# Optimization experiments

Hardware: AMD Instinct MI355X
Metric: run time of the kernel (lower is better)

## Reference

```python
import jax, jax.numpy as jnp
import numpy as np

D = 256; NH = 8; HD = D // NH; FF = 1024; NLAYERS = 6
REG_MAX = 32; NBIN = REG_MAX + 1; NC = 80; KQ = 4
SPATIAL = [(80, 80), (40, 40), (20, 20)]; NPTS = [4, 4, 4]; SUMP = sum(NPTS)
LQ = 300; B = 16; OFFSET_SCALE = 0.5; UP = 0.5; REG_SCALE = 4.0
TOT = NH * SUMP


def _project_np():
    ub1 = abs(UP) * abs(REG_SCALE); ub2 = ub1 * 2
    step = (ub1 + 1.0) ** (2.0 / (REG_MAX - 2))
    left = [-(step ** i) + 1 for i in range(REG_MAX // 2 - 1, 0, -1)]
    right = [step ** i - 1 for i in range(1, REG_MAX // 2)]
    return np.array([-ub2] + left + [0.0] + right + [ub2], dtype=np.float32)

PROJ_NP = _project_np()  # [NBIN]


def layer_norm(x, g, b):
    mu = x.mean(-1, keepdims=True)
    var = ((x - mu) ** 2).mean(-1, keepdims=True)
    return (x - mu) * jax.lax.rsqrt(var + 1e-5) * g + b


def inv_sigmoid(x, eps=1e-5):
    x = jnp.clip(x, eps, 1.0 - eps)
    return jnp.log(x) - jnp.log1p(-x)


def mlp2(x, w1, b1, w2, b2):
    return jax.nn.silu(x @ w1 + b1) @ w2 + b2


def mlp3(x, w1, b1, w2, b2, w3, b3):
    return jax.nn.silu(jax.nn.silu(x @ w1 + b1) @ w2 + b2) @ w3 + b3


def grid_sample(img, grid):
    # bilinear, padding_mode='zeros', align_corners=False. img [N,C,H,W], grid [N,Hg,Wg,2] in [-1,1]
    N, C, H, W = img.shape
    gshape = grid.shape[1:3]
    x = (grid[..., 0] + 1.0) * (W * 0.5) - 0.5
    y = (grid[..., 1] + 1.0) * (H * 0.5) - 0.5
    x0f = jnp.floor(x); y0f = jnp.floor(y)
    wx = x - x0f; wy = y - y0f
    x0 = x0f.astype(jnp.int32); y0 = y0f.astype(jnp.int32)
    imgf = img.reshape(N, C, H * W)
    def tap(xi, yi, wt):
        valid = ((xi >= 0) & (xi < W) & (yi >= 0) & (yi < H)).astype(img.dtype)
        idx = jnp.clip(yi, 0, H - 1) * W + jnp.clip(xi, 0, W - 1)
        v = jnp.take_along_axis(imgf, idx.reshape(N, 1, -1), axis=2).reshape(N, C, gshape[0], gshape[1])
        return v * (valid * wt)[:, None]
    return (tap(x0, y0, (1 - wx) * (1 - wy)) + tap(x0 + 1, y0, wx * (1 - wy))
            + tap(x0, y0 + 1, (1 - wx) * wy) + tap(x0 + 1, y0 + 1, wx * wy))


def self_attention(q_in, k_in, v_in, qw, qb, kw, kb, vw, vb, ow, ob):
    q = (q_in @ qw + qb).reshape(B, LQ, NH, HD)
    k = (k_in @ kw + kb).reshape(B, LQ, NH, HD)
    v = (v_in @ vw + vb).reshape(B, LQ, NH, HD)
    a = jax.nn.softmax(jnp.einsum('bqhd,bkhd->bhqk', q, k) * (HD ** -0.5), -1)
    o = jnp.einsum('bhqk,bkhd->bqhd', a, v).reshape(B, LQ, D)
    return o @ ow + ob


def distance2bbox(points, distance):
    rs = abs(REG_SCALE); half = 0.5 * rs
    x1 = points[..., 0] - (half + distance[..., 0]) * (points[..., 2] / rs)
    y1 = points[..., 1] - (half + distance[..., 1]) * (points[..., 3] / rs)
    x2 = points[..., 0] + (half + distance[..., 2]) * (points[..., 2] / rs)
    y2 = points[..., 1] + (half + distance[..., 3]) * (points[..., 3] / rs)
    return jnp.stack([(x1 + x2) * 0.5, (y1 + y2) * 0.5, x2 - x1, y2 - y1], -1)


def lqe_head(scores, corners, w1, b1, w2, b2):
    prob = jax.nn.softmax(corners.reshape(B, LQ, 4, NBIN), -1)
    topk, _ = jax.lax.top_k(prob, KQ)                         # [B,LQ,4,KQ]
    stat = jnp.concatenate([topk, topk.mean(-1, keepdims=True)], -1)  # [B,LQ,4,KQ+1]
    return scores + mlp2(stat.reshape(B, LQ, 4 * (KQ + 1)), w1, b1, w2, b2)


def reference(target, ref_pts_unact, memory,
              sa_qw, sa_qb, sa_kw, sa_kb, sa_vw, sa_vb, sa_ow, sa_ob,
              n1_g, n1_b, off_w, off_b, aw_w, aw_b,
              gate_w, gate_b, gn_g, gn_b,
              ff1_w, ff1_b, ff2_w, ff2_b, n3_g, n3_b,
              bb_w1, bb_b1, bb_w2, bb_b2, bb_w3, bb_b3,
              sc_w, sc_b, lqe_w1, lqe_b1, lqe_w2, lqe_b2,
              qp_w1, qp_b1, qp_w2, qp_b2,
              pb_w1, pb_b1, pb_w2, pb_b2, pb_w3, pb_b3):
    project = jnp.asarray(PROJ_NP)
    # --- value prep: memory [B,S,D] -> per-level [B*NH, HD, h, w] ---
    val = memory.reshape(B, -1, NH, HD).transpose(0, 2, 3, 1).reshape(B * NH, HD, -1)
    splits = np.cumsum([h * w for h, w in SPATIAL])[:-1].tolist()
    value_lvls = [v.reshape(B * NH, HD, h, w)
                  for v, (h, w) in zip(jnp.split(val, splits, axis=2), SPATIAL)]
    nps = jnp.asarray(np.repeat(1.0 / np.array(NPTS, np.float32), NPTS))  # [SUMP]

    ref_pts = jax.nn.sigmoid(ref_pts_unact)
    output = target
    out_prev = jnp.zeros_like(target)
    corners_prev = jnp.zeros((B, LQ, 4 * NBIN), dtype=target.dtype)
    ref_init = ref_pts
    final_logits = final_bboxes = None

    for i in range(NLAYERS):
        qp = jnp.clip(mlp2(ref_pts, qp_w1, qp_b1, qp_w2, qp_b2), -10.0, 10.0)
        # self attention
        q = output + qp
        t2 = self_attention(q, q, output, sa_qw[i], sa_qb[i], sa_kw[i], sa_kb[i],
                            sa_vw[i], sa_vb[i], sa_ow[i], sa_ob[i])
        output = layer_norm(output + t2, n1_g[i], n1_b[i])
        # deformable cross attention
        qc = output + qp
        offs = (qc @ off_w[i] + off_b[i]).reshape(B, LQ, NH, SUMP, 2)
        attnw = jax.nn.softmax((qc @ aw_w[i] + aw_b[i]).reshape(B, LQ, NH, SUMP), -1)
        offset = offs * nps[:, None] * ref_pts[:, :, None, None, 2:] * OFFSET_SCALE
        locs = ref_pts[:, :, None, None, :2] + offset            # [B,LQ,NH,SUMP,2]
        grids = (2.0 * locs - 1.0).transpose(0, 2, 1, 3, 4).reshape(B * NH, LQ, SUMP, 2)
        p0 = 0; sampled = []
        for lvl in range(len(SPATIAL)):
            sampled.append(grid_sample(value_lvls[lvl], grids[:, :, p0:p0 + NPTS[lvl]]))
            p0 += NPTS[lvl]
        samp = jnp.concatenate(sampled, -1)                      # [B*NH, HD, LQ, SUMP]
        aw = attnw.transpose(0, 2, 1, 3).reshape(B * NH, 1, LQ, SUMP)
        t2 = (samp * aw).sum(-1).reshape(B, D, LQ).transpose(0, 2, 1)
        # gateway
        g12 = jax.nn.sigmoid(jnp.concatenate([output, t2], -1) @ gate_w[i] + gate_b[i])
        output = layer_norm(g12[..., :D] * output + g12[..., D:] * t2, gn_g[i], gn_b[i])
        # FFN
        t2 = jax.nn.relu(output @ ff1_w[i] + ff1_b[i]) @ ff2_w[i] + ff2_b[i]
        output = layer_norm(jnp.clip(output + t2, -65504.0, 65504.0), n3_g[i], n3_b[i])
        # FDR box refinement
        if i == 0:
            pre_bb = jax.nn.sigmoid(mlp3(output, pb_w1, pb_b1, pb_w2, pb_b2, pb_w3, pb_b3)
                                    + inv_sigmoid(ref_pts))
            ref_init = pre_bb
        corners = mlp3(output + out_prev, bb_w1[i], bb_b1[i], bb_w2[i], bb_b2[i],
                       bb_w3[i], bb_b3[i]) + corners_prev
        dist = jax.nn.softmax(corners.reshape(B, LQ, 4, NBIN), -1) @ project  # [B,LQ,4]
        inter = distance2bbox(ref_init, dist)
        if i == NLAYERS - 1:  # eval_idx
            scores = output @ sc_w[i] + sc_b[i]
            final_logits = lqe_head(scores, corners, lqe_w1[i], lqe_b1[i], lqe_w2[i], lqe_b2[i])
            final_bboxes = inter
        corners_prev = corners
        ref_pts = inter
        out_prev = output
    return jnp.concatenate([final_bboxes, final_logits], -1)  # [B, LQ, 4+NC]


def setup_inputs() -> dict:
    key = jax.random.key(0)
    cnt = [0]
    def rnd(shape, scale=0.02):
        cnt[0] += 1
        return jax.random.normal(jax.random.fold_in(key, cnt[0]), shape, dtype=jnp.float32) * scale
    S = sum(h * w for h, w in SPATIAL)
    L = NLAYERS
    return {
        'target': rnd((B, LQ, D), 1.0),
        'ref_pts_unact': rnd((B, LQ, 4), 1.0),
        'memory': rnd((B, S, D), 1.0),
        'sa_qw': rnd((L, D, D)), 'sa_qb': rnd((L, D)),
        'sa_kw': rnd((L, D, D)), 'sa_kb': rnd((L, D)),
        'sa_vw': rnd((L, D, D)), 'sa_vb': rnd((L, D)),
        'sa_ow': rnd((L, D, D)), 'sa_ob': rnd((L, D)),
        'n1_g': jnp.ones((L, D)), 'n1_b': jnp.zeros((L, D)),
        'off_w': rnd((L, D, TOT * 2)), 'off_b': rnd((L, TOT * 2)),
        'aw_w': rnd((L, D, TOT)), 'aw_b': rnd((L, TOT)),
        'gate_w': rnd((L, 2 * D, 2 * D)), 'gate_b': rnd((L, 2 * D)),
        'gn_g': jnp.ones((L, D)), 'gn_b': jnp.zeros((L, D)),
        'ff1_w': rnd((L, D, FF)), 'ff1_b': rnd((L, FF)),
        'ff2_w': rnd((L, FF, D)), 'ff2_b': rnd((L, D)),
        'n3_g': jnp.ones((L, D)), 'n3_b': jnp.zeros((L, D)),
        'bb_w1': rnd((L, D, D)), 'bb_b1': rnd((L, D)),
        'bb_w2': rnd((L, D, D)), 'bb_b2': rnd((L, D)),
        'bb_w3': rnd((L, D, 4 * NBIN)), 'bb_b3': rnd((L, 4 * NBIN)),
        'sc_w': rnd((L, D, NC)), 'sc_b': rnd((L, NC)),
        'lqe_w1': rnd((L, 4 * (KQ + 1), 64)), 'lqe_b1': rnd((L, 64)),
        'lqe_w2': rnd((L, 64, 1)), 'lqe_b2': rnd((L, 1)),
        'qp_w1': rnd((4, 2 * D)), 'qp_b1': rnd((2 * D,)),
        'qp_w2': rnd((2 * D, D)), 'qp_b2': rnd((D,)),
        'pb_w1': rnd((D, D)), 'pb_b1': rnd((D,)),
        'pb_w2': rnd((D, D)), 'pb_b2': rnd((D,)),
        'pb_w3': rnd((D, 4)), 'pb_b3': rnd((4,)),
    }
```

## Files before the change

### kernel.cpp

```cpp
#include <hip/hip_runtime.h>
#include <cstddef>
#include <cmath>
#include <utility>

#define B_ 16
#define LQ_ 300
#define D_ 256
#define NH_ 8
#define HD_ 32
#define FF_ 1024
#define NBIN_ 33
#define NC_ 80
#define SUMP_ 12
#define STOT_ 8400
#define R_ (B_*LQ_)
#define NLAYERS_ 6

typedef short bf16x8 __attribute__((ext_vector_type(8)));
typedef float f32x4  __attribute__((ext_vector_type(4)));

static __device__ __forceinline__ short f2bf(float x) {
  union { float f; unsigned u; } v; v.f = x;
  unsigned r = v.u + 0x7fffu + ((v.u >> 16) & 1u);
  return (short)(r >> 16);
// ... 155 lines not shown
      bf16x8 ab0 = *(const bf16x8*)(obp0 + k0 + lq * 8);
      bf16x8 ab1 = *(const bf16x8*)(obp1 + k0 + lq * 8);
      #pragma unroll
      for (int t = 0; t < 6; ++t) {
        bf16x8 w = *(const bf16x8*)(Qt + (size_t)(cbase + t * 16 + lr) * 256 + k0 + lq * 8);
        bool useoq = (cbase + t * 16) < 512;
        acc[0][t] = __builtin_amdgcn_mfma_f32_16x16x32_bf16(useoq ? aq0 : ab0, w, acc[0][t], 0, 0, 0);
        acc[1][t] = __builtin_amdgcn_mfma_f32_16x16x32_bf16(useoq ? aq1 : ab1, w, acc[1][t], 0, 0, 0);
      }
    }
    #pragma unroll
    for (int t = 0; t < 6; ++t) {
      int colt = cbase + t * 16 + lr;
      float bv = qkvbias[colt];
      #pragma unroll
      for (int ti = 0; ti < 2; ++ti)
        #pragma unroll
        for (int rr = 0; rr < 4; ++rr)
          qkvout[(size_t)(m0 + ti * 16 + lq * 4 + rr) * 768 + colt] = f2bf(acc[ti][t][rr] + bv);
    }
  }
}

__launch_bounds__(512)
__global__ void sow_ln_off(const short* __restrict__ A, const short* __restrict__ Wt,
                           const float* __restrict__ bias, const float* __restrict__ resid,
                           const float* __restrict__ gamma, const float* __restrict__ beta,
                           const float* __restrict__ qp,
                           const short* __restrict__ OWt, const float* __restrict__ ob,
                           float* __restrict__ outf, short* __restrict__ outbf,
                           float* __restrict__ offout) {
  __shared__ float ssum[32][8];
  __shared__ float ssq[32][8];
  __shared__ short oqs[32][264];
  const int m0 = blockIdx.x * 32;
  const int tid = threadIdx.x, wid = tid >> 6, lane = tid & 63;
  const int lr = lane & 15, lq = lane >> 4;
  const int cw = wid * 32;
  f32x4 acc[2][2];
  #pragma unroll
  for (int ti = 0; ti < 2; ++ti)
    #pragma unroll
    for (int t = 0; t < 2; ++t) acc[ti][t] = (f32x4){0.f, 0.f, 0.f, 0.f};
  #pragma unroll
  for (int k0 = 0; k0 < 256; k0 += 32) {
    bf16x8 a0 = *(const bf16x8*)(A + (size_t)(m0 + lr) * 256 + k0 + lq * 8);
    bf16x8 a1 = *(const bf16x8*)(A + (size_t)(m0 + 16 + lr) * 256 + k0 + lq * 8);
    #pragma unroll
    for (int t = 0; t < 2; ++t) {
      bf16x8 w = *(const bf16x8*)(Wt + (size_t)(cw + t * 16 + lr) * 256 + k0 + lq * 8);
      acc[0][t] = __builtin_amdgcn_mfma_f32_16x16x32_bf16(a0, w, acc[0][t], 0, 0, 0);
      acc[1][t] = __builtin_amdgcn_mfma_f32_16x16x32_bf16(a1, w, acc[1][t], 0, 0, 0);
    }
  }
  float s[2][4], q[2][4];
  #pragma unroll
  for (int ti = 0; ti < 2; ++ti)
    #pragma unroll
    for (int rr = 0; rr < 4; ++rr) { s[ti][rr] = 0.f; q[ti][rr] = 0.f; }
  #pragma unroll
  for (int t = 0; t < 2; ++t) {
    int col = cw + t * 16 + lr;
    float bv = bias[col];
    #pragma unroll
    for (int ti = 0; ti < 2; ++ti)
      #pragma unroll
      for (int rr = 0; rr < 4; ++rr) {
        int rowg = m0 + ti * 16 + lq * 4 + rr;
        float x = acc[ti][t][rr] + bv + resid[(size_t)rowg * 256 + col];
        acc[ti][t][rr] = x;
        s[ti][rr] += x; q[ti][rr] += x * x;
      }
  }
  #pragma unroll
  for (int m = 1; m < 16; m <<= 1)
    #pragma unroll
    for (int ti = 0; ti < 2; ++ti)
      #pragma unroll
      for (int rr = 0; rr < 4; ++rr) {
        s[ti][rr] += __shfl_xor(s[ti][rr], m);
        q[ti][rr] += __shfl_xor(q[ti][rr], m);
      }
  if (lr == 0)
    #pragma unroll
    for (int ti = 0; ti < 2; ++ti)
      #pragma unroll
      for (int rr = 0; rr < 4; ++rr) {
        ssum[ti * 16 + lq * 4 + rr][wid] = s[ti][rr];
        ssq[ti * 16 + lq * 4 + rr][wid] = q[ti][rr];
      }
  __syncthreads();
  float mu[2][4], rs[2][4];
  #pragma unroll
  for (int ti = 0; ti < 2; ++ti)
    #pragma unroll
    for (int rr = 0; rr < 4; ++rr) {
      int rl = ti * 16 + lq * 4 + rr;
      float sm = 0.f, sq = 0.f;
      #pragma unroll
      for (int w8 = 0; w8 < 8; ++w8) { sm += ssum[rl][w8]; sq += ssq[rl][w8]; }
      float m_ = sm * (1.f / 256.f);
      float var = sq * (1.f / 256.f) - m_ * m_;
      mu[ti][rr] = m_; rs[ti][rr] = rsqrtf(var + 1e-5f);
    }
  #pragma unroll
  for (int t = 0; t < 2; ++t) {
    int col = cw + t * 16 + lr;
    float g = gamma[col], be = beta[col];
    #pragma unroll
    for (int ti = 0; ti < 2; ++ti)
      #pragma unroll
      for (int rr = 0; rr < 4; ++rr) {
        int rl = ti * 16 + lq * 4 + rr;
        size_t idx = (size_t)(m0 + rl) * 256 + col;
        float v = (acc[ti][t][rr] - mu[ti][rr]) * rs[ti][rr] * g + be;
        outf[idx] = v;
        outbf[idx] = f2bf(v);
        oqs[rl][col] = f2bf(v + qp[idx]);
      }
  }
  __syncthreads();
  f32x4 oacc[2][3];
  #pragma unroll
  for (int ti = 0; ti < 2; ++ti)
    #pragma unroll
    for (int j = 0; j < 3; ++j) oacc[ti][j] = (f32x4){0.f, 0.f, 0.f, 0.f};
  #pragma unroll 4
  for (int k0 = 0; k0 < 256; k0 += 32) {
    bf16x8 a0 = *(const bf16x8*)&oqs[lr][k0 + lq * 8];
    bf16x8 a1 = *(const bf16x8*)&oqs[16 + lr][k0 + lq * 8];
    #pragma unroll
    for (int j = 0; j < 3; ++j) {
      int tile = wid + j * 8;
      int trow = (tile < 18) ? tile * 16 + lr : 0;
      bf16x8 w = *(const bf16x8*)(OWt + (size_t)trow * 256 + k0 + lq * 8);
      oacc[0][j] = __builtin_amdgcn_mfma_f32_16x16x32_bf16(a0, w, oacc[0][j], 0, 0, 0);
      oacc[1][j] = __builtin_amdgcn_mfma_f32_16x16x32_bf16(a1, w, oacc[1][j], 0, 0, 0);
    }
  }
  #pragma unroll
  for (int j = 0; j < 3; ++j) {
    int tile = wid + j * 8;
    if (tile >= 18) continue;
    int col = tile * 16 + lr;
    float bv = ob[col];
    #pragma unroll
    for (int ti = 0; ti < 2; ++ti)
      #pragma unroll
      for (int rr = 0; rr < 4; ++rr)
        offout[(size_t)(m0 + ti * 16 + lq * 4 + rr) * 288 + col] = oacc[ti][j][rr] + bv;
  }
}

template<int SCORES>
__launch_bounds__(512)
__global__ void ffn_ln(const short* __restrict__ A, const short* __restrict__ W1t,
                       const float* __restrict__ b1, const short* __restrict__ W2t,
                       const float* __restrict__ b2, const float* __restrict__ resid,
                       const float* __restrict__ gamma, const float* __restrict__ beta,
                       float* __restrict__ prev, float* __restrict__ outf,
                       short* __restrict__ outbf, short* __restrict__ oqbf,
                       const short* __restrict__ SCt, const float* __restrict__ scb,
                       float* __restrict__ scoresOut) {
  __shared__ short hid[32][1032];
  __shared__ float ssum[32][8];
  __shared__ float ssq[32][8];
  const int m0 = blockIdx.x * 32;
  const int tid = threadIdx.x, wid = tid >> 6, lane = tid & 63;
  const int lr = lane & 15, lq = lane >> 4;
  {
    f32x4 acc[2][8];
    #pragma unroll
    for (int ti = 0; ti < 2; ++ti)
      #pragma unroll
      for (int t = 0; t < 8; ++t) acc[ti][t] = (f32x4){0.f, 0.f, 0.f, 0.f};
    #pragma unroll 4
    for (int k0 = 0; k0 < 256; k0 += 32) {
      bf16x8 a0 = *(const bf16x8*)(A + (size_t)(m0 + lr) * 256 + k0 + lq * 8);
      bf16x8 a1 = *(const bf16x8*)(A + (size_t)(m0 + 16 + lr) * 256 + k0 + lq * 8);
      #pragma unroll
      for (int t = 0; t < 8; ++t) {
        bf16x8 w = *(const bf16x8*)(W1t + (size_t)(wid * 128 + t * 16 + lr) * 256 + k0 + lq * 8);
        acc[0][t] = __builtin_amdgcn_mfma_f32_16x16x32_bf16(a0, w, acc[0][t], 0, 0, 0);
        acc[1][t] = __builtin_amdgcn_mfma_f32_16x16x32_bf16(a1, w, acc[1][t], 0, 0, 0);
      }
    }
    #pragma unroll
    for (int t = 0; t < 8; ++t) {
      int col = wid * 128 + t * 16 + lr;
      float bv = b1[col];
      #pragma unroll
      for (int ti = 0; ti < 2; ++ti)
        #pragma unroll
        for (int rr = 0; rr < 4; ++rr)
          hid[ti * 16 + lq * 4 + rr][col] = f2bf(fmaxf(acc[ti][t][rr] + bv, 0.f));
    }
  }
  __syncthreads();
  const int cw = wid * 32;
  f32x4 acc[2][2];
  #pragma unroll
  for (int ti = 0; ti < 2; ++ti)
    #pragma unroll
    for (int t = 0; t < 2; ++t) acc[ti][t] = (f32x4){0.f, 0.f, 0.f, 0.f};
  #pragma unroll 8
  for (int k0 = 0; k0 < 1024; k0 += 32) {
    bf16x8 a0 = *(const bf16x8*)&hid[lr][k0 + lq * 8];
    bf16x8 a1 = *(const bf16x8*)&hid[16 + lr][k0 + lq * 8];
    #pragma unroll
    for (int t = 0; t < 2; ++t) {
      bf16x8 w = *(const bf16x8*)(W2t + (size_t)(cw + t * 16 + lr) * 1024 + k0 + lq * 8);
      acc[0][t] = __builtin_amdgcn_mfma_f32_16x16x32_bf16(a0, w, acc[0][t], 0, 0, 0);
      acc[1][t] = __builtin_amdgcn_mfma_f32_16x16x32_bf16(a1, w, acc[1][t], 0, 0, 0);
    }
  }
  float s[2][4], q[2][4];
  #pragma unroll
  for (int ti = 0; ti < 2; ++ti)
    #pragma unroll
    for (int rr = 0; rr < 4; ++rr) { s[ti][rr] = 0.f; q[ti][rr] = 0.f; }
  #pragma unroll
  for (int t = 0; t < 2; ++t) {
    int col = cw + t * 16 + lr;
    float bv = b2[col];
    #pragma unroll
    for (int ti = 0; ti < 2; ++ti)
      #pragma unroll
      for (int rr = 0; rr < 4; ++rr) {
        int rowg = m0 + ti * 16 + lq * 4 + rr;
        float x = acc[ti][t][rr] + bv + resid[(size_t)rowg * 256 + col];
        x = fminf(fmaxf(x, -65504.f), 65504.f);
        acc[ti][t][rr] = x;
        s[ti][rr] += x; q[ti][rr] += x * x;
      }
  }
  #pragma unroll
  for (int m = 1; m < 16; m <<= 1)
    #pragma unroll
    for (int ti = 0; ti < 2; ++ti)
      #pragma unroll
      for (int rr = 0; rr < 4; ++rr) {
        s[ti][rr] += __shfl_xor(s[ti][rr], m);
        q[ti][rr] += __shfl_xor(q[ti][rr], m);
      }
  if (lr == 0)
    #pragma unroll
    for (int ti = 0; ti < 2; ++ti)
      #pragma unroll
      for (int rr = 0; rr < 4; ++rr) {
        ssum[ti * 16 + lq * 4 + rr][wid] = s[ti][rr];
        ssq[ti * 16 + lq * 4 + rr][wid] = q[ti][rr];
      }
  __syncthreads();
  float mu[2][4], rs[2][4];
  #pragma unroll
  for (int ti = 0; ti < 2; ++ti)
    #pragma unroll
    for (int rr = 0; rr < 4; ++rr) {
      int rl = ti * 16 + lq * 4 + rr;
      float sm = 0.f, sq = 0.f;
      #pragma unroll
      for (int w8 = 0; w8 < 8; ++w8) { sm += ssum[rl][w8]; sq += ssq[rl][w8]; }
      float m_ = sm * (1.f / 256.f);
      float var = sq * (1.f / 256.f) - m_ * m_;
      mu[ti][rr] = m_; rs[ti][rr] = rsqrtf(var + 1e-5f);
    }
  #pragma unroll
  for (int t = 0; t < 2; ++t) {
    int col = cw + t * 16 + lr;
    float g = gamma[col], be = beta[col];
    #pragma unroll
    for (int ti = 0; ti < 2; ++ti)
      #pragma unroll
      for (int rr = 0; rr < 4; ++rr) {
        int rl = ti * 16 + lq * 4 + rr;
        size_t idx = (size_t)(m0 + rl) * 256 + col;
        float v = (acc[ti][t][rr] - mu[ti][rr]) * rs[ti][rr] * g + be;
        outf[idx] = v;
        short vb = f2bf(v);
        outbf[idx] = vb;
        float po = prev[idx];
        oqbf[idx] = f2bf(v + po);
        prev[idx] = v;
        if (SCORES) hid[rl][col] = vb;
      }
  }
  if (SCORES) {
    __syncthreads();
    f32x4 sacc[2];
    sacc[0] = (f32x4){0.f, 0.f, 0.f, 0.f};
    sacc[1] = (f32x4){0.f, 0.f, 0.f, 0.f};
    int trow = (wid < 5) ? wid * 16 + lr : 0;
    #pragma unroll 4
    for (int k0 = 0; k0 < 256; k0 += 32) {
      bf16x8 a0 = *(const bf16x8*)&hid[lr][k0 + lq * 8];
      bf16x8 a1 = *(const bf16x8*)&hid[16 + lr][k0 + lq * 8];
      bf16x8 w = *(const bf16x8*)(SCt + (size_t)trow * 256 + k0 + lq * 8);
      sacc[0] = __builtin_amdgcn_mfma_f32_16x16x32_bf16(a0, w, sacc[0], 0, 0, 0);
      sacc[1] = __builtin_amdgcn_mfma_f32_16x16x32_bf16(a1, w, sacc[1], 0, 0, 0);
    }
    if (wid < 5) {
      int col = wid * 16 + lr;
      float bv = scb[col];
      #pragma unroll
      for (int ti = 0; ti < 2; ++ti)
        #pragma unroll
        for (int rr = 0; rr < 4; ++rr)
          scoresOut[(size_t)(m0 + ti * 16 + lq * 4 + rr) * 80 + col] = sacc[ti][rr] + bv;
    }
  }
}

template<int LQE>
__launch_bounds__(512)
__global__ void fdr_kernel(const short* __restrict__ A,
                           const short* __restrict__ W1t, const float* __restrict__ b1,
                           const short* __restrict__ W2t, const float* __restrict__ b2,
                           const short* __restrict__ W3t, const float* __restrict__ b3,
                           const float* __restrict__ cprev, const float* __restrict__ refi,
                           float* __restrict__ ccur, float* __restrict__ refn,
                           const float* __restrict__ scores, const float* __restrict__ lw1,
                           const float* __restrict__ lb1, const float* __restrict__ lw2,
                           const float* __restrict__ lb2, float* __restrict__ outp) {
  __shared__ short h1[32][264];
  __shared__ short h2[32][264];
  __shared__ float cor[32][132];
  __shared__ float dstl[32][4];
  __shared__ float projs[33];
  __shared__ float statl[32][20];
  __shared__ float interb[32][4];
  __shared__ float lqes[32];
  const int m0 = blockIdx.x * 32;
  const int tid = threadIdx.x, wid = tid >> 6, lane = tid & 63;
  const int lr = lane & 15, lq = lane >> 4;
  if (tid < 33) {
    float v;
    if (tid == 0) v = -4.f;
    else if (tid == 32) v = 4.f;
    else if (tid == 16) v = 0.f;
    else if (tid < 16) v = 1.f - powf(3.f, (float)(16 - tid) * (1.f / 15.f));
    else v = powf(3.f, (float)(tid - 16) * (1.f / 15.f)) - 1.f;
    projs[tid] = v;
  }
  {
    f32x4 acc[2][2];
    #pragma unroll
    for (int ti = 0; ti < 2; ++ti)
      #pragma unroll
      for (int t = 0; t < 2; ++t) acc[ti][t] = (f32x4){0.f, 0.f, 0.f, 0.f};
    #pragma unroll
    for (int k0 = 0; k0 < 256; k0 += 32) {
      bf16x8 a0 = *(const bf16x8*)(A + (size_t)(m0 + lr) * 256 + k0 + lq * 8);
      bf16x8 a1 = *(const bf16x8*)(A + (size_t)(m0 + 16 + lr) * 256 + k0 + lq * 8);
      #pragma unroll
      for (int t = 0; t < 2; ++t) {
        bf16x8 w = *(const bf16x8*)(W1t + (size_t)(wid * 32 + t * 16 + lr) * 256 + k0 + lq * 8);
        acc[0][t] = __builtin_amdgcn_mfma_f32_16x16x32_bf16(a0, w, acc[0][t], 0, 0, 0);
        acc[1][t] = __builtin_amdgcn_mfma_f32_16x16x32_bf16(a1, w, acc[1][t], 0, 0, 0);
      }
    }
    #pragma unroll
    for (int t = 0; t < 2; ++t) {
      int col = wid * 32 + t * 16 + lr;
      float bv = b1[col];
      #pragma unroll
      for (int ti = 0; ti < 2; ++ti)
        #pragma unroll
        for (int rr = 0; rr < 4; ++rr) {
          float v = acc[ti][t][rr] + bv;
          v = v / (1.f + __expf(-v));
          h1[ti * 16 + lq * 4 + rr][col] = f2bf(v);
        }
    }
  }
  __syncthreads();
  {
    f32x4 acc[2][2];
    #pragma unroll
    for (int ti = 0; ti < 2; ++ti)
      #pragma unroll
      for (int t = 0; t < 2; ++t) acc[ti][t] = (f32x4){0.f, 0.f, 0.f, 0.f};
    #pragma unroll
    for (int k0 = 0; k0 < 256; k0 += 32) {
      bf16x8 a0 = *(const bf16x8*)&h1[lr][k0 + lq * 8];
      bf16x8 a1 = *(const bf16x8*)&h1[16 + lr][k0 + lq * 8];
      #pragma unroll
      for (int t = 0; t < 2; ++t) {
        bf16x8 w = *(const bf16x8*)(W2t + (size_t)(wid * 32 + t * 16 + lr) * 256 + k0 + lq * 8);
        acc[0][t] = __builtin_amdgcn_mfma_f32_16x16x32_bf16(a0, w, acc[0][t], 0, 0, 0);
        acc[1][t] = __builtin_amdgcn_mfma_f32_16x16x32_bf16(a1, w, acc[1][t], 0, 0, 0);
      }
    }
    #pragma unroll
    for (int t = 0; t < 2; ++t) {
      int col = wid * 32 + t * 16 + lr;
      float bv = b2[col];
      #pragma unroll
      for (int ti = 0; ti < 2; ++ti)
        #pragma unroll
        for (int rr = 0; rr < 4; ++rr) {
          float v = acc[ti][t][rr] + bv;
          v = v / (1.f + __expf(-v));
          h2[ti * 16 + lq * 4 + rr][col] = f2bf(v);
        }
    }
  }
  __syncthreads();
  {
    f32x4 acc[2][2];
    int col[2], wr[2];
    #pragma unroll
    for (int j = 0; j < 2; ++j) {
      acc[0][j] = (f32x4){0.f, 0.f, 0.f, 0.f};
      acc[1][j] = (f32x4){0.f, 0.f, 0.f, 0.f};
      col[j] = (wid + j * 8) * 16 + lr;
      wr[j] = (col[j] < 132) ? col[j] : 0;
    }
    #pragma unroll
    for (int k0 = 0; k0 < 256; k0 += 32) {
      bf16x8 a0 = *(const bf16x8*)&h2[lr][k0 + lq * 8];
      bf16x8 a1 = *(const bf16x8*)&h2[16 + lr][k0 + lq * 8];
      #pragma unroll
      for (int j = 0; j < 2; ++j) {
        bf16x8 w = *(const bf16x8*)(W3t + (size_t)wr[j] * 256 + k0 + lq * 8);
        acc[0][j] = __builtin_amdgcn_mfma_f32_16x16x32_bf16(a0, w, acc[0][j], 0, 0, 0);
        acc[1][j] = __builtin_amdgcn_mfma_f32_16x16x32_bf16(a1, w, acc[1][j], 0, 0, 0);
      }
    }
    #pragma unroll
    for (int j = 0; j < 2; ++j) {
      if (col[j] >= 132) continue;
      float bv = b3[col[j]];
      #pragma unroll
      for (int ti = 0; ti < 2; ++ti)
        #pragma unroll
        for (int rr = 0; rr < 4; ++rr) {
          int rl = ti * 16 + lq * 4 + rr, g = m0 + rl;
          float v = acc[ti][j][rr] + bv + cprev[(size_t)g * 132 + col[j]];
          ccur[(size_t)g * 132 + col[j]] = v;
          cor[rl][col[j]] = v;
        }
    }
  }
  __syncthreads();
  if (tid < 128) {
    int r = tid >> 2, sd = tid & 3;
    const float* cp = &cor[r][sd * 33];
    float m = -1e30f;
    #pragma unroll
// ... 305 lines not shown
    for (int r = 0; r < 4; ++r) {
      int q = q0 + lq * 4 + r;
      if (q >= 300) continue;
      float inv = 1.f / l[r];
      size_t ob = (size_t)(b * LQ_ + q) * 256 + h * 32;
      O[ob + lr]      = f2bf(o0[r] * inv);
      O[ob + 16 + lr] = f2bf(o1[r] * inv);
    }
  }
}

template<int BF16MEM>
__launch_bounds__(512)
__global__ void deform_kernel(const void* __restrict__ memv, const float* __restrict__ offaw,
                              const float* __restrict__ refp,
                              float* __restrict__ t2, short* __restrict__ t2bf) {
  const int bi = blockIdx.x;
  const int tid = threadIdx.x;
  const int sub = tid >> 8;
  const int row = (bi & 7) * 600 + (bi >> 3) * 2 + sub;
  const int b = row / LQ_;
  const int it = tid & 255;
  const int h = it >> 5, c = it & 31;
  const float rx = refp[row * 4 + 0], ry = refp[row * 4 + 1];
  const float rw = refp[row * 4 + 2], rh = refp[row * 4 + 3];
  const float* awp = offaw + (size_t)row * 288 + 192 + h * SUMP_;
  float wv[SUMP_];
  float wmax = -1e30f;
  #pragma unroll
  for (int p = 0; p < SUMP_; ++p) { wv[p] = awp[p]; wmax = fmaxf(wmax, wv[p]); }
  float wsum = 0.f;
  #pragma unroll
  for (int p = 0; p < SUMP_; ++p) { wv[p] = __expf(wv[p] - wmax); wsum += wv[p]; }
  const float winv = 1.f / wsum;
  const float* op = offaw + (size_t)row * 288 + h * (SUMP_ * 2);
  const short* mb16 = BF16MEM ? ((const short*)memv + ((size_t)(b * 8 + h) * STOT_) * 32 + c) : nullptr;
  const float* mb32 = BF16MEM ? nullptr : ((const float*)memv + (size_t)b * STOT_ * 256 + h * 32 + c);
  float acc = 0.f;
  #pragma unroll
  for (int p = 0; p < SUMP_; ++p) {
    const int lvl = p >> 2;
    const int Wl = (lvl == 0) ? 80 : ((lvl == 1) ? 40 : 20);
    const int s0 = (lvl == 0) ? 0 : ((lvl == 1) ? 6400 : 8000);
    float lx = rx + op[2 * p]     * 0.125f * rw;
    float ly = ry + op[2 * p + 1] * 0.125f * rh;
    float x = lx * Wl - 0.5f, y = ly * Wl - 0.5f;
    float xf = floorf(x), yf = floorf(y);
    int x0 = (int)xf, y0 = (int)yf;
    float wx = x - xf, wy = y - yf;
    int x0c = min(max(x0, 0), Wl - 1), x1c = min(max(x0 + 1, 0), Wl - 1);
    int y0c = min(max(y0, 0), Wl - 1), y1c = min(max(y0 + 1, 0), Wl - 1);
    float wx0 = (x0 >= 0 && x0 < Wl) ? (1.f - wx) : 0.f;
    float wx1 = (x0 + 1 >= 0 && x0 + 1 < Wl) ? wx : 0.f;
    float wy0 = (y0 >= 0 && y0 < Wl) ? (1.f - wy) : 0.f;
    float wy1 = (y0 + 1 >= 0 && y0 + 1 < Wl) ? wy : 0.f;
    float v;
    if (BF16MEM) {
      const short* mb = mb16 + (size_t)s0 * 32;
      v = wx0 * wy0 * bf2f(mb[(size_t)(y0c * Wl + x0c) * 32])
        + wx1 * wy0 * bf2f(mb[(size_t)(y0c * Wl + x1c) * 32])
        + wx0 * wy1 * bf2f(mb[(size_t)(y1c * Wl + x0c) * 32])
        + wx1 * wy1 * bf2f(mb[(size_t)(y1c * Wl + x1c) * 32]);
    } else {
      const float* mb = mb32 + (size_t)s0 * 256;
      v = wx0 * wy0 * mb[(size_t)(y0c * Wl + x0c) * 256]
        + wx1 * wy0 * mb[(size_t)(y0c * Wl + x1c) * 256]
        + wx0 * wy1 * mb[(size_t)(y1c * Wl + x0c) * 256]
        + wx1 * wy1 * mb[(size_t)(y1c * Wl + x1c) * 256];
    }
    acc += wv[p] * winv * v;
  }
  size_t off = (size_t)row * D_ + h * HD_ + c;
  t2[off] = acc;
  t2bf[off] = f2bf(acc);
}

static inline dim3 egrid(int n) { return dim3((n + 255) / 256); }

extern "C" void kernel_launch(void* const* d_in, const int* in_sizes, int n_in,
                              void* d_out, int out_size, void* d_ws, size_t ws_size,
                              hipStream_t stream) {
  const float* target     = (const float*)d_in[0];
  const float* ref_unact  = (const float*)d_in[1];
  const float* memory     = (const float*)d_in[2];
  const float* sa_qw = (const float*)d_in[3];  const float* sa_qb = (const float*)d_in[4];
  const float* sa_kw = (const float*)d_in[5];  const float* sa_kb = (const float*)d_in[6];
  const float* sa_vw = (const float*)d_in[7];  const float* sa_vb = (const float*)d_in[8];
  const float* sa_ow = (const float*)d_in[9];  const float* sa_ob = (const float*)d_in[10];
  const float* n1_g  = (const float*)d_in[11]; const float* n1_b  = (const float*)d_in[12];
  const float* off_w = (const float*)d_in[13]; const float* off_b = (const float*)d_in[14];
  const float* aw_w  = (const float*)d_in[15]; const float* aw_b  = (const float*)d_in[16];
  const float* gate_w= (const float*)d_in[17]; const float* gate_b= (const float*)d_in[18];
  const float* gn_g  = (const float*)d_in[19]; const float* gn_b  = (const float*)d_in[20];
  const float* ff1_w = (const float*)d_in[21]; const float* ff1_b = (const float*)d_in[22];
  const float* ff2_w = (const float*)d_in[23]; const float* ff2_b = (const float*)d_in[24];
  const float* n3_g  = (const float*)d_in[25]; const float* n3_b  = (const float*)d_in[26];
  const float* bb_w1 = (const float*)d_in[27]; const float* bb_b1 = (const float*)d_in[28];
  const float* bb_w2 = (const float*)d_in[29]; const float* bb_b2 = (const float*)d_in[30];
  const float* bb_w3 = (const float*)d_in[31]; const float* bb_b3 = (const float*)d_in[32];
  const float* sc_w  = (const float*)d_in[33]; const float* sc_b  = (const float*)d_in[34];
  const float* lqe_w1= (const float*)d_in[35]; const float* lqe_b1= (const float*)d_in[36];
  const float* lqe_w2= (const float*)d_in[37]; const float* lqe_b2= (const float*)d_in[38];
  const float* qp_w1 = (const float*)d_in[39]; const float* qp_b1 = (const float*)d_in[40];
  const float* qp_w2 = (const float*)d_in[41]; const float* qp_b2 = (const float*)d_in[42];
  const float* pb_w1 = (const float*)d_in[43]; const float* pb_b1 = (const float*)d_in[44];
  const float* pb_w2 = (const float*)d_in[45]; const float* pb_b2 = (const float*)d_in[46];
  const float* pb_w3 = (const float*)d_in[47]; const float* pb_b3 = (const float*)d_in[48];
  float* out = (float*)d_out;

  float* ws = (float*)d_ws;
  size_t woff = 0;
  auto alloc = [&](size_t n) { float* p = ws + woff; woff += n; return p; };
  float* output   = alloc((size_t)R_ * D_);
  float* out_prev = alloc((size_t)R_ * D_);
  float* qp       = alloc((size_t)R_ * D_);
  float* t2       = alloc((size_t)R_ * D_);
  float* offawf   = alloc((size_t)R_ * 288);
  float* U        = alloc((size_t)R_ * 512);
  float* corners0 = alloc((size_t)R_ * 4 * NBIN_);
  float* corners1 = alloc((size_t)R_ * 4 * NBIN_);
  float* refA     = alloc((size_t)R_ * 4);
  float* refB     = alloc((size_t)R_ * 4);
  float* ref_init = alloc((size_t)R_ * 4);
  float* qkvb     = alloc((size_t)NLAYERS_ * 768);
  float* offawb   = alloc((size_t)NLAYERS_ * 288);

  short* sws = (short*)(ws + woff);
  size_t soff = 0;
  auto salloc = [&](size_t n) { short* p = sws + soff; soff += n; return p; };
  short* outbf = salloc((size_t)R_ * D_);
  short* oqbf  = salloc((size_t)R_ * D_);
  short* tbf   = salloc((size_t)R_ * D_);
  short* qp2t  = salloc((size_t)256 * 512);
  short* sqkvt = salloc((size_t)NLAYERS_ * 768 * 256);
  short* sowt  = salloc((size_t)NLAYERS_ * 256 * 256);
  short* soffawt = salloc((size_t)NLAYERS_ * 288 * 256);
  short* gatet = salloc((size_t)NLAYERS_ * 512 * 512);
  short* ff1t  = salloc((size_t)NLAYERS_ * 1024 * 256);
  short* ff2t  = salloc((size_t)NLAYERS_ * 256 * 1024);
  short* bb1t  = salloc((size_t)NLAYERS_ * 256 * 256);
  short* bb2t  = salloc((size_t)NLAYERS_ * 256 * 256);
  short* bb3t  = salloc((size_t)NLAYERS_ * 132 * 256);
  short* pb1t  = salloc((size_t)256 * 256);
  short* pb2t  = salloc((size_t)256 * 256);
  short* pb3t  = salloc((size_t)4 * 256);
  short* sct   = salloc((size_t)80 * 256);
  size_t base_bytes = woff * sizeof(float) + soff * sizeof(short);
  if (ws_size < base_bytes) return;
  const size_t memn = (size_t)B_ * STOT_ * 256;
  bool bf16mem = (ws_size >= base_bytes + memn * sizeof(short));
  short* membf = sws + soff;

  short* qkv    = (short*)U;
  float* scores = offawf;

  float* c_prev = corners0; float* c_cur = corners1;
  float* ref_cur = refA;    float* ref_nxt = refB;

  WJobs P; int nb = 0; int nj = 0;
  auto addj = [&](const float* s, short* d2, int K, int N, int L, int ostr) {
    P.j[nj].src = s; P.j[nj].dst = d2; P.j[nj].K = K; P.j[nj].N = N;
    P.j[nj].tk = (K + 31) / 32; P.j[nj].tn = (N + 31) / 32;
    P.j[nj].L = L; P.j[nj].ostride = ostr; P.j[nj].blk0 = nb; P.j[nj].pad = 0;
    nb += P.j[nj].tk * P.j[nj].tn * L; ++nj;
  };
  addj(qp_w2, qp2t, 512, 256, 1, 512 * 256);
  addj(sa_qw, sqkvt,               256, 256, NLAYERS_, 768 * 256);
  addj(sa_kw, sqkvt + 256 * 256,   256, 256, NLAYERS_, 768 * 256);
  addj(sa_vw, sqkvt + 512 * 256,   256, 256, NLAYERS_, 768 * 256);
  addj(sa_ow, sowt, 256, 256, NLAYERS_, 256 * 256);
  addj(off_w, soffawt,             256, 192, NLAYERS_, 288 * 256);
  addj(aw_w,  soffawt + 192 * 256, 256,  96, NLAYERS_, 288 * 256);
  addj(gate_w, gatet, 512, 512, NLAYERS_, 512 * 512);
  addj(ff1_w, ff1t, 256, 1024, NLAYERS_, 1024 * 256);
  addj(ff2_w, ff2t, 1024, 256, NLAYERS_, 256 * 1024);
  addj(bb_w1, bb1t, 256, 256, NLAYERS_, 256 * 256);
  addj(bb_w2, bb2t, 256, 256, NLAYERS_, 256 * 256);
  addj(bb_w3, bb3t, 256, 132, NLAYERS_, 132 * 256);
  addj(pb_w1, pb1t, 256, 256, 1, 256 * 256);
  addj(pb_w2, pb2t, 256, 256, 1, 256 * 256);
  addj(pb_w3, pb3t, 256, 4, 1, 4 * 256);
  addj(sc_w + (size_t)5 * D_ * NC_, sct, 256, 80, 1, 80 * 256);
  P.njobs = nj;
  wconv_all<<<dim3(nb), 256, 0, stream>>>(P);
  if (bf16mem)
    memconv_kernel<<<dim3(B_ * STOT_ / 4), 256, 0, stream>>>(memory, membf);

  misc_init<<<egrid(R_ * 64), 256, 0, stream>>>(target, ref_unact,
      sa_qb, sa_kb, sa_vb, off_b, aw_b,
      output, outbf, out_prev, c_prev, ref_cur, qkvb, offawb);

  for (int i = 0; i < NLAYERS_; ++i) {
    qp_qkv<<<dim3(150), 512, 0, stream>>>(ref_cur, qp_w1, qp_b1, qp2t, qp_b2,
                                          output, outbf,
                                          sqkvt + (size_t)i * 768 * 256,
                                          qkvb + (size_t)i * 768, qp, qkv);
    attn3_kernel<<<dim3(B_ * NH_ * 2), 256, 0, stream>>>(qkv, tbf);
    sow_ln_off<<<dim3(150), 512, 0, stream>>>(
        tbf, sowt + (size_t)i * 65536, sa_ob + (size_t)i * D_, output,
        n1_g + (size_t)i * D_, n1_b + (size_t)i * D_, qp,
        soffawt + (size_t)i * 288 * 256, offawb + (size_t)i * 288,
        output, outbf, offawf);

    if (bf16mem)
      deform_kernel<1><<<dim3(R_ / 2), 512, 0, stream>>>(membf, offawf, ref_cur, t2, tbf);
    else
      deform_kernel<0><<<dim3(R_ / 2), 512, 0, stream>>>(memory, offawf, ref_cur, t2, tbf);

    gate_ln<<<dim3(150), 512, 0, stream>>>(outbf, tbf, gatet + (size_t)i * 262144,
                                           gate_b + (size_t)i * 512, t2,
                                           gn_g + (size_t)i * D_, gn_b + (size_t)i * D_,
                                           output, outbf);

    if (i < NLAYERS_ - 1)
      ffn_ln<0><<<dim3(150), 512, 0, stream>>>(outbf, ff1t + (size_t)i * 262144,
          ff1_b + (size_t)i * FF_, ff2t + (size_t)i * 262144, ff2_b + (size_t)i * D_,
          output, n3_g + (size_t)i * D_, n3_b + (size_t)i * D_,
          out_prev, output, outbf, oqbf, nullptr, nullptr, nullptr);
    else
      ffn_ln<1><<<dim3(150), 512, 0, stream>>>(outbf, ff1t + (size_t)i * 262144,
          ff1_b + (size_t)i * FF_, ff2t + (size_t)i * 262144, ff2_b + (size_t)i * D_,
          output, n3_g + (size_t)i * D_, n3_b + (size_t)i * D_,
          out_prev, output, outbf, oqbf, sct, sc_b + (size_t)5 * NC_, scores);

    if (i == 0)
      pb_fused<<<dim3(150), 512, 0, stream>>>(outbf, pb1t, pb_b1, pb2t, pb_b2,
                                              pb3t, pb_b3, ref_cur, ref_init);
    if (i < NLAYERS_ - 1) {
      fdr_kernel<0><<<dim3(150), 512, 0, stream>>>(oqbf,
          bb1t + (size_t)i * 65536, bb_b1 + (size_t)i * D_,
          bb2t + (size_t)i * 65536, bb_b2 + (size_t)i * D_,
          bb3t + (size_t)i * 33792, bb_b3 + (size_t)i * 4 * NBIN_,
          c_prev, ref_init, c_cur, ref_nxt,
          nullptr, nullptr, nullptr, nullptr, nullptr, nullptr);
      std::swap(c_prev, c_cur);
      std::swap(ref_cur, ref_nxt);
    } else {
      fdr_kernel<1><<<dim3(150), 512, 0, stream>>>(oqbf,
          bb1t + (size_t)i * 65536, bb_b1 + (size_t)i * D_,
          bb2t + (size_t)i * 65536, bb_b2 + (size_t)i * D_,
          bb3t + (size_t)i * 33792, bb_b3 + (size_t)i * 4 * NBIN_,
          c_prev, ref_init, c_cur, ref_nxt,
          scores, lqe_w1 + (size_t)5 * 20 * 64, lqe_b1 + (size_t)5 * 64,
          lqe_w2 + (size_t)5 * 64, lqe_b2 + (size_t)5, out);
    }
  }
}
```

Before: 1.645 ms.

## Split fused FFN into separate FF1 GEMM kernel and FF2+LayerNorm kernel

The FFN's first GEMM moves out of the fused kernel into its own ff1_gemm launch over a 4x75 grid, which writes the bf16 hidden activations to a global scratch buffer. The FF2+LayerNorm kernel then reads the hidden tile from global memory instead of shared memory. The goal is to raise parallelism for the FF1 stage, since the fused kernel had only 150 blocks each doing a 32x1024 GEMM, and to shrink shared-memory use. The cost is an extra launch per layer and a round trip of the 4800x1024 hidden tensor through global memory, plus reuse of the qkv scratch buffer U, which must be large enough to hold it.

```diff
diff --git a/kernel.cpp b/kernel.cpp
--- a/kernel.cpp
+++ b/kernel.cpp
@@ -331,51 +331,63 @@
   }
 }
 
+__launch_bounds__(512)
+__global__ void ff1_gemm(const short* __restrict__ A, const short* __restrict__ W1t,
+                         const float* __restrict__ b1, short* __restrict__ hid) {
+  const int ct = blockIdx.x;
+  const int m0 = blockIdx.y * 64;
+  const int tid = threadIdx.x, wid = tid >> 6, lane = tid & 63;
+  const int lr = lane & 15, lq = lane >> 4;
+  const int cb = ct * 256 + wid * 32;
+  f32x4 acc[4][2];
+  #pragma unroll
+  for (int ti = 0; ti < 4; ++ti)
+    #pragma unroll
+    for (int t = 0; t < 2; ++t) acc[ti][t] = (f32x4){0.f, 0.f, 0.f, 0.f};
+  #pragma unroll
+  for (int k0 = 0; k0 < 256; k0 += 32) {
+    bf16x8 a0 = *(const bf16x8*)(A + (size_t)(m0 + lr) * 256 + k0 + lq * 8);
+    bf16x8 a1 = *(const bf16x8*)(A + (size_t)(m0 + 16 + lr) * 256 + k0 + lq * 8);
+    bf16x8 a2 = *(const bf16x8*)(A + (size_t)(m0 + 32 + lr) * 256 + k0 + lq * 8);
+    bf16x8 a3 = *(const bf16x8*)(A + (size_t)(m0 + 48 + lr) * 256 + k0 + lq * 8);
+    #pragma unroll
+    for (int t = 0; t < 2; ++t) {
+      bf16x8 w = *(const bf16x8*)(W1t + (size_t)(cb + t * 16 + lr) * 256 + k0 + lq * 8);
+      acc[0][t] = __builtin_amdgcn_mfma_f32_16x16x32_bf16(a0, w, acc[0][t], 0, 0, 0);
+      acc[1][t] = __builtin_amdgcn_mfma_f32_16x16x32_bf16(a1, w, acc[1][t], 0, 0, 0);
+      acc[2][t] = __builtin_amdgcn_mfma_f32_16x16x32_bf16(a2, w, acc[2][t], 0, 0, 0);
+      acc[3][t] = __builtin_amdgcn_mfma_f32_16x16x32_bf16(a3, w, acc[3][t], 0, 0, 0);
+    }
+  }
+  #pragma unroll
+  for (int t = 0; t < 2; ++t) {
+    int col = cb + t * 16 + lr;
+    float bv = b1[col];
+    #pragma unroll
+    for (int ti = 0; ti < 4; ++ti)
+      #pragma unroll
+      for (int rr = 0; rr < 4; ++rr) {
+        int rowg = m0 + ti * 16 + lq * 4 + rr;
+        hid[(size_t)rowg * 1024 + col] = f2bf(fmaxf(acc[ti][t][rr] + bv, 0.f));
+      }
+  }
+}
+
 template<int SCORES>
 __launch_bounds__(512)
-__global__ void ffn_ln(const short* __restrict__ A, const short* __restrict__ W1t,
-                       const float* __restrict__ b1, const short* __restrict__ W2t,
-                       const float* __restrict__ b2, const float* __restrict__ resid,
-                       const float* __restrict__ gamma, const float* __restrict__ beta,
-                       float* __restrict__ prev, float* __restrict__ outf,
-                       short* __restrict__ outbf, short* __restrict__ oqbf,
-                       const short* __restrict__ SCt, const float* __restrict__ scb,
-                       float* __restrict__ scoresOut) {
-  __shared__ short hid[32][1032];
+__global__ void ffn2_ln(const short* __restrict__ H, const short* __restrict__ W2t,
+                        const float* __restrict__ b2, const float* __restrict__ resid,
+                        const float* __restrict__ gamma, const float* __restrict__ beta,
+                        float* __restrict__ prev, float* __restrict__ outf,
+                        short* __restrict__ outbf, short* __restrict__ oqbf,
+                        const short* __restrict__ SCt, const float* __restrict__ scb,
+                        float* __restrict__ scoresOut) {
   __shared__ float ssum[32][8];
   __shared__ float ssq[32][8];
+  __shared__ short sbuf[32][264];
   const int m0 = blockIdx.x * 32;
   const int tid = threadIdx.x, wid = tid >> 6, lane = tid & 63;
   const int lr = lane & 15, lq = lane >> 4;
-  {
-    f32x4 acc[2][8];
-    #pragma unroll
-    for (int ti = 0; ti < 2; ++ti)
-      #pragma unroll
-      for (int t = 0; t < 8; ++t) acc[ti][t] = (f32x4){0.f, 0.f, 0.f, 0.f};
-    #pragma unroll 4
-    for (int k0 = 0; k0 < 256; k0 += 32) {
-      bf16x8 a0 = *(const bf16x8*)(A + (size_t)(m0 + lr) * 256 + k0 + lq * 8);
-      bf16x8 a1 = *(const bf16x8*)(A + (size_t)(m0 + 16 + lr) * 256 + k0 + lq * 8);
-      #pragma unroll
-      for (int t = 0; t < 8; ++t) {
-        bf16x8 w = *(const bf16x8*)(W1t + (size_t)(wid * 128 + t * 16 + lr) * 256 + k0 + lq * 8);
-        acc[0][t] = __builtin_amdgcn_mfma_f32_16x16x32_bf16(a0, w, acc[0][t], 0, 0, 0);
-        acc[1][t] = __builtin_amdgcn_mfma_f32_16x16x32_bf16(a1, w, acc[1][t], 0, 0, 0);
-      }
-    }
-    #pragma unroll
-    for (int t = 0; t < 8; ++t) {
-      int col = wid * 128 + t * 16 + lr;
-      float bv = b1[col];
-      #pragma unroll
-      for (int ti = 0; ti < 2; ++ti)
-        #pragma unroll
-        for (int rr = 0; rr < 4; ++rr)
-          hid[ti * 16 + lq * 4 + rr][col] = f2bf(fmaxf(acc[ti][t][rr] + bv, 0.f));
-    }
-  }
-  __syncthreads();
   const int cw = wid * 32;
   f32x4 acc[2][2];
   #pragma unroll
@@ -384,8 +396,8 @@
     for (int t = 0; t < 2; ++t) acc[ti][t] = (f32x4){0.f, 0.f, 0.f, 0.f};
   #pragma unroll 8
   for (int k0 = 0; k0 < 1024; k0 += 32) {
-    bf16x8 a0 = *(const bf16x8*)&hid[lr][k0 + lq * 8];
-    bf16x8 a1 = *(const bf16x8*)&hid[16 + lr][k0 + lq * 8];
+    bf16x8 a0 = *(const bf16x8*)(H + (size_t)(m0 + lr) * 1024 + k0 + lq * 8);
+    bf16x8 a1 = *(const bf16x8*)(H + (size_t)(m0 + 16 + lr) * 1024 + k0 + lq * 8);
     #pragma unroll
     for (int t = 0; t < 2; ++t) {
       bf16x8 w = *(const bf16x8*)(W2t + (size_t)(cw + t * 16 + lr) * 1024 + k0 + lq * 8);
@@ -461,7 +473,7 @@
         float po = prev[idx];
         oqbf[idx] = f2bf(v + po);
         prev[idx] = v;
-        if (SCORES) hid[rl][col] = vb;
+        if (SCORES) sbuf[rl][col] = vb;
       }
   }
   if (SCORES) {
@@ -472,8 +484,8 @@
     int trow = (wid < 5) ? wid * 16 + lr : 0;
     #pragma unroll 4
     for (int k0 = 0; k0 < 256; k0 += 32) {
-      bf16x8 a0 = *(const bf16x8*)&hid[lr][k0 + lq * 8];
-      bf16x8 a1 = *(const bf16x8*)&hid[16 + lr][k0 + lq * 8];
+      bf16x8 a0 = *(const bf16x8*)&sbuf[lr][k0 + lq * 8];
+      bf16x8 a1 = *(const bf16x8*)&sbuf[16 + lr][k0 + lq * 8];
       bf16x8 w = *(const bf16x8*)(SCt + (size_t)trow * 256 + k0 + lq * 8);
       sacc[0] = __builtin_amdgcn_mfma_f32_16x16x32_bf16(a0, w, sacc[0], 0, 0, 0);
       sacc[1] = __builtin_amdgcn_mfma_f32_16x16x32_bf16(a1, w, sacc[1], 0, 0, 0);
@@ -1085,6 +1097,7 @@
   short* membf = sws + soff;
 
   short* qkv    = (short*)U;
+  short* hidbf  = (short*)U;
   float* scores = offawf;
 
   float* c_prev = corners0; float* c_cur = corners1;
@@ -1145,14 +1158,16 @@
                                            gn_g + (size_t)i * D_, gn_b + (size_t)i * D_,
                                            output, outbf);
 
+    ff1_gemm<<<dim3(4, 75), 512, 0, stream>>>(outbf, ff1t + (size_t)i * 262144,
+                                              ff1_b + (size_t)i * FF_, hidbf);
     if (i < NLAYERS_ - 1)
-      ffn_ln<0><<<dim3(150), 512, 0, stream>>>(outbf, ff1t + (size_t)i * 262144,
-          ff1_b + (size_t)i * FF_, ff2t + (size_t)i * 262144, ff2_b + (size_t)i * D_,
+      ffn2_ln<0><<<dim3(150), 512, 0, stream>>>(hidbf,
+          ff2t + (size_t)i * 262144, ff2_b + (size_t)i * D_,
           output, n3_g + (size_t)i * D_, n3_b + (size_t)i * D_,
           out_prev, output, outbf, oqbf, nullptr, nullptr, nullptr);
     else
-      ffn_ln<1><<<dim3(150), 512, 0, stream>>>(outbf, ff1t + (size_t)i * 262144,
-          ff1_b + (size_t)i * FF_, ff2t + (size_t)i * 262144, ff2_b + (size_t)i * D_,
+      ffn2_ln<1><<<dim3(150), 512, 0, stream>>>(hidbf,
+          ff2t + (size_t)i * 262144, ff2_b + (size_t)i * D_,
           output, n3_g + (size_t)i * D_, n3_b + (size_t)i * D_,
           out_prev, output, outbf, oqbf, sct, sc_b + (size_t)5 * NC_, scores);
 
```

Result: slower. 1.678 ms (+2.0%).
